# Performance work log

Measured on AMD Instinct MI355X. Metric: run time of the kernel, lower is better.

The kernel has to match this reference:

```python
import jax, jax.numpy as jnp
import numpy as np
from jax import lax

S, B, V, E, H = 512, 64, 50000, 400, 1150


def _lstm_layer(x, h0, c0, Wih, Whh, bih, bhh):
    # x: [S, B, Din]; PyTorch LSTM gate order: i, f, g, o
    WihT, WhhT = Wih.T, Whh.T

    def step(carry, xt):
        h, c = carry
        gates = xt @ WihT + bih + h @ WhhT + bhh  # [B, 4*Dh]
        i, f, g, o = jnp.split(gates, 4, axis=-1)
        c_new = jax.nn.sigmoid(f) * c + jax.nn.sigmoid(i) * jnp.tanh(g)
        h_new = jax.nn.sigmoid(o) * jnp.tanh(c_new)
        return (h_new, c_new), h_new

    (_, _), ys = lax.scan(step, (h0, c0), x)
    return ys  # [S, B, Dh]


def setup_inputs() -> dict:
    key = jax.random.key(0)

    def u(i, shape, s):
        return jax.random.uniform(jax.random.fold_in(key, i), shape, jnp.float32, -s, s)

    inp = {"tokens": jax.random.randint(jax.random.fold_in(key, 0), (S, B), 0, V)}
    inp["emb_w"] = u(1, (V, E), 0.1)  # encoder.weight.uniform_(-0.1, 0.1)
    dims = [(E, H), (H, H), (H, E)]  # (input_size, hidden_size) per layer
    k = 2
    for l, (din, dh) in enumerate(dims):
        s = 1.0 / float(np.sqrt(dh))
        inp[f"Wih{l}"] = u(k, (4 * dh, din), s); k += 1
        inp[f"Whh{l}"] = u(k, (4 * dh, dh), s); k += 1
        inp[f"bih{l}"] = u(k, (4 * dh,), s); k += 1
        inp[f"bhh{l}"] = u(k, (4 * dh,), s); k += 1
        inp[f"h{l}"] = jnp.zeros((B, dh), jnp.float32)
        inp[f"c{l}"] = jnp.zeros((B, dh), jnp.float32)
    return inp


def reference(tokens, emb_w, Wih0, Whh0, bih0, bhh0, Wih1, Whh1, bih1, bhh1,
              Wih2, Whh2, bih2, bhh2, h0, c0, h1, c1, h2, c2):
    # Eval-mode forward: embedding/locked/weight dropouts are identity.
    x = emb_w[tokens]  # [S, B, E]
    x = _lstm_layer(x, h0, c0, Wih0, Whh0, bih0, bhh0)  # [S, B, H]
    x = _lstm_layer(x, h1, c1, Wih1, Whh1, bih1, bhh1)  # [S, B, H]
    x = _lstm_layer(x, h2, c2, Wih2, Whh2, bih2, bhh2)  # [S, B, E]
    return x
```

## Files before the change

kernel.cpp:

```cpp
#include <hip/hip_runtime.h>
#include <hip/hip_bf16.h>
#include <cstdint>
#include <cstddef>


typedef _Float16 f16x8 __attribute__((ext_vector_type(8)));
typedef float f32x4 __attribute__((ext_vector_type(4)));
typedef unsigned int u32x4 __attribute__((ext_vector_type(4)));

#define LSTM_NBLK   241
#define LSTM_WSTEPS 515
#define LDS_W_HALFS (4 * 36 * 64 * 8)
#define LDS_TOTAL_BYTES (LDS_W_HALFS * 2 + 16384)
#define GO_BASE 248

struct KParams {
  const unsigned short* res[3];
  const unsigned short* strm[3];
  const float* bias[3];
  const unsigned short* xin0;
  unsigned short* hseq[3];
  float* part;
  float* out;
  int* bar;
};

__device__ __forceinline__ float sigm_(float x) { return 1.0f / (1.0f + __expf(-x)); }
__device__ __forceinline__ float tanh_(float x) { return 2.0f * sigm_(2.0f * x) - 1.0f; }
__device__ __forceinline__ unsigned short f2h(float x) {
  _Float16 h = (_Float16)x;
  return __builtin_bit_cast(unsigned short, h);
}
__device__ __forceinline__ f32x4 load_sc128f(const float* p) {
  f32x4 r;
  asm volatile("global_load_dwordx4 %0, %1, off sc0 sc1"
               : "=v"(r) : "v"(p) : "memory");
  return r;
}
__device__ __forceinline__ void store_sc128(unsigned short* p, u32x4 v) {
  asm volatile("global_store_dwordx4 %0, %1, off sc0 sc1" :: "v"(p), "v"(v) : "memory");
}
__device__ __forceinline__ void store_sc128f(float* p, f32x4 v) {
  asm volatile("global_store_dwordx4 %0, %1, off sc0 sc1" :: "v"(p), "v"(v) : "memory");
}
__device__ __forceinline__ void store_sc_i(int* p, int v) {
  asm volatile("global_store_dword %0, %1, off sc0 sc1" :: "v"(p), "v"(v) : "memory");
}
__device__ __forceinline__ int load_sc_i(const int* p) {
  int v;
  asm volatile("global_load_dword %0, %1, off sc0 sc1\n\ts_waitcnt vmcnt(0)"
               : "=v"(v) : "v"(p) : "memory");
  __builtin_amdgcn_sched_barrier(0);
  return v;
}
__device__ __forceinline__ void wait_vm0() {
  asm volatile("s_waitcnt vmcnt(0)" ::: "memory");
  __builtin_amdgcn_sched_barrier(0);
}

__device__ __forceinline__ void grid_barrier(int* bar, int bid, int tid, int tau1) {
  wait_vm0();
  __syncthreads();
  if (bid == 0) {
    if (tid >= 1 && tid < LSTM_NBLK) {
      int guard = 0;
      while (load_sc_i(&bar[tid * 32]) < tau1 && ++guard < (1 << 20))
        __builtin_amdgcn_s_sleep(1);
    }
    __syncthreads();
    if (tid < 8) store_sc_i(&bar[(GO_BASE + tid) * 32], tau1);
  } else {
    if (tid == 0) {
      store_sc_i(&bar[bid * 32], tau1);
      int guard = 0;
      while (load_sc_i(&bar[(GO_BASE + (bid & 7)) * 32]) < tau1 && ++guard < (1 << 20))
        __builtin_amdgcn_s_sleep(1);
    }
    __syncthreads();
  }
}

template<int L, int LAG>
__device__ __forceinline__ void run_layer(const KParams& p, int g, int bid,
                                          unsigned short* ldsW, float* gates) {
  constexpr int DH    = (L == 2) ? 400 : 1150;
  constexpr int NKB1  = (L == 0) ? 13 : 36;
  constexpr int NKB2  = (L == 2) ? 13 : 36;
  constexpr int XSTR  = (L == 0) ? 416 : 1152;
  constexpr int HSTR  = (L == 2) ? 416 : 1152;
  constexpr bool B1_RES = (L == 2);
  constexpr int NKB_ST = B1_RES ? NKB2 : NKB1;

  const unsigned short* __restrict__ strm = p.strm[L] + (size_t)g * (4 * NKB_ST * 512);
  const float* __restrict__ bias          = p.bias[L];
  const unsigned short* __restrict__ xin  = (L == 0) ? p.xin0 : p.hseq[L - 1];
  unsigned short* __restrict__ own        = p.hseq[L];

  const int tid  = threadIdx.x;
  const int lane = tid & 63;
  const int w    = tid >> 6;
  const int m0   = (w >> 2) << 4;
  const int kq   = w & 3;
  const int r    = lane & 15;
  const int q    = lane >> 4;

  {
    const uint4* src = (const uint4*)(p.res[L] + (size_t)g * LDS_W_HALFS);
    uint4* dst = (uint4*)ldsW;
    for (int i = tid; i < LDS_W_HALFS / 8; i += 1024) dst[i] = src[i];
#pragma unroll
    for (int s2 = 0; s2 < 4; ++s2) gates[s2 * 1024 + tid] = 0.0f;
  }

  const int b_ = tid >> 4;
  const int jp = tid & 15;
  const int jglob = g * 16 + jp;
  float bias4[4];
#pragma unroll
  for (int ss = 0; ss < 4; ++ss) bias4[ss] = bias[ss * 1152 + jglob];
  float c_val = 0.0f;
  __syncthreads();

  for (int tau = 0; tau < LSTM_WSTEPS; ++tau) {
    const int t = tau - LAG;
    if (t >= 0 && t < 512) {
      f32x4 acc[4] = {{0,0,0,0},{0,0,0,0},{0,0,0,0},{0,0,0,0}};

      const size_t slot1 = (L == 0) ? (size_t)t : (size_t)(t + 1);
      const unsigned short* a1base = xin + slot1 * (64 * XSTR) + (size_t)(m0 + r) * XSTR + q * 8;
      const unsigned short* a2base = own + (size_t)t * (64 * HSTR) + (size_t)(m0 + r) * HSTR + q * 8;

      f16x8 a1r[9]; f16x8 a2r[9];
      if constexpr (L != 0) {
#pragma unroll
        for (int i = 0; i < 9; ++i) {
          int kb = kq + 4 * i;
          if (NKB1 == 36 || kb < NKB1) a1r[i] = *(const f16x8*)(a1base + kb * 32);
        }
      }
#pragma unroll
      for (int i = 0; i < 9; ++i) {
        int kb = kq + 4 * i;
        if (i < ((NKB2 == 36) ? 9 : 4) && (NKB2 == 36 || kb < NKB2))
          a2r[i] = *(const f16x8*)(a2base + kb * 32);
      }

#pragma unroll
      for (int i = 0; i < ((NKB1 == 36) ? 9 : 4); ++i) {
        int kb = kq + 4 * i;
        if (NKB1 == 36 || kb < NKB1) {
          f16x8 a = (L == 0) ? *(const f16x8*)(a1base + kb * 32) : a1r[i];
#pragma unroll
          for (int s2 = 0; s2 < 4; ++s2) {
            f16x8 b = B1_RES
              ? *(const f16x8*)&ldsW[((s2 * 36 + kb) * 64 + lane) * 8]
              : *(const f16x8*)&strm[((size_t)(s2 * NKB_ST + kb) * 64 + lane) * 8];
            acc[s2] = __builtin_amdgcn_mfma_f32_16x16x32_f16(a, b, acc[s2], 0, 0, 0);
          }
        }
      }
#pragma unroll
      for (int i = 0; i < ((NKB2 == 36) ? 9 : 4); ++i) {
        int kb = kq + 4 * i;
        if (NKB2 == 36 || kb < NKB2) {
          f16x8 a = a2r[i];
#pragma unroll
          for (int s2 = 0; s2 < 4; ++s2) {
            f16x8 b = B1_RES
              ? *(const f16x8*)&strm[((size_t)(s2 * NKB_ST + kb) * 64 + lane) * 8]
              : *(const f16x8*)&ldsW[((s2 * 36 + kb) * 64 + lane) * 8];
            acc[s2] = __builtin_amdgcn_mfma_f32_16x16x32_f16(a, b, acc[s2], 0, 0, 0);
          }
        }
      }

#pragma unroll
      for (int s2 = 0; s2 < 4; ++s2)
#pragma unroll
        for (int i = 0; i < 4; ++i)
          atomicAdd(&gates[s2 * 1024 + (m0 + q * 4 + i) * 16 + r], acc[s2][i]);
      __syncthreads();

      float pg[4];
#pragma unroll
      for (int s2 = 0; s2 < 4; ++s2) {
        pg[s2] = gates[s2 * 1024 + tid];
        gates[s2 * 1024 + tid] = 0.0f;
      }
      float ig = sigm_(pg[0] + bias4[0]);
      float fg = sigm_(pg[1] + bias4[1]);
      float gg = tanh_(pg[2] + bias4[2]);
      float og = sigm_(pg[3] + bias4[3]);
      c_val = fg * c_val + ig * gg;
      float h = og * tanh_(c_val);
      if (jglob >= DH) h = 0.0f;

      unsigned v0  = (unsigned)f2h(h);
      unsigned o1  = __shfl_down(v0, 1);
      unsigned p01 = v0 | (o1 << 16);
      unsigned o2  = __shfl_down(p01, 2);
      unsigned o4a = __shfl_down(p01, 4);
      unsigned o4b = __shfl_down(o2, 4);
      if ((lane & 7) == 0) {
        u32x4 pk; pk[0] = p01; pk[1] = o2; pk[2] = o4a; pk[3] = o4b;
        store_sc128(own + ((size_t)(t + 1) * 64 + b_) * HSTR + jglob, pk);
      }
      if (L == 2 && jglob < DH)
        p.out[((size_t)t * 64 + b_) * 400 + jglob] = h;
    }
    grid_barrier(p.bar, bid, tid, tau + 1);
  }
}

__device__ __forceinline__ void run_l1_ih(const KParams& p, int g, int bid,
                                          unsigned short* ldsW, float* gates) {
  const unsigned short* __restrict__ xin = p.hseq[0];
  const int tid  = threadIdx.x;
  const int lane = tid & 63;
  const int w    = tid >> 6;
  const int m0   = (w >> 2) << 4;
  const int kq   = w & 3;
  const int r    = lane & 15;
  const int q    = lane >> 4;

  {
    const uint4* src = (const uint4*)(p.strm[1] + (size_t)g * LDS_W_HALFS);
    uint4* dst = (uint4*)ldsW;
    for (int i = tid; i < LDS_W_HALFS / 8; i += 1024) dst[i] = src[i];
#pragma unroll
    for (int s2 = 0; s2 < 4; ++s2) gates[s2 * 1024 + tid] = 0.0f;
  }
  __syncthreads();

  for (int tau = 0; tau < LSTM_WSTEPS; ++tau) {
    const int t = tau - 1;
    if (t >= 0 && t < 512) {
      f32x4 acc[4] = {{0,0,0,0},{0,0,0,0},{0,0,0,0},{0,0,0,0}};
      const unsigned short* a1base =
          xin + (size_t)(t + 1) * (64 * 1152) + (size_t)(m0 + r) * 1152 + q * 8;
      f16x8 a1r[9];
#pragma unroll
      for (int i = 0; i < 9; ++i) a1r[i] = *(const f16x8*)(a1base + (kq + 4 * i) * 32);
#pragma unroll
      for (int i = 0; i < 9; ++i) {
        int kb = kq + 4 * i;
        f16x8 a = a1r[i];
#pragma unroll
        for (int s2 = 0; s2 < 4; ++s2) {
          f16x8 b = *(const f16x8*)&ldsW[((s2 * 36 + kb) * 64 + lane) * 8];
          acc[s2] = __builtin_amdgcn_mfma_f32_16x16x32_f16(a, b, acc[s2], 0, 0, 0);
        }
      }
#pragma unroll
      for (int s2 = 0; s2 < 4; ++s2)
#pragma unroll
        for (int i = 0; i < 4; ++i)
          atomicAdd(&gates[s2 * 1024 + (m0 + q * 4 + i) * 16 + r], acc[s2][i]);
      __syncthreads();
      f32x4 pk;
#pragma unroll
      for (int s2 = 0; s2 < 4; ++s2) {
        pk[s2] = gates[s2 * 1024 + tid];
        gates[s2 * 1024 + tid] = 0.0f;
      }
      store_sc128f(p.part + ((size_t)((t & 1) * 72 + g) * 1024 + tid) * 4, pk);
    }
    grid_barrier(p.bar, bid, tid, tau + 1);
  }
}

__device__ __forceinline__ void run_l1_hh(const KParams& p, int g, int bid,
                                          unsigned short* ldsW, float* gates) {
  unsigned short* __restrict__ own = p.hseq[1];
  const int tid  = threadIdx.x;
  const int lane = tid & 63;
  const int w    = tid >> 6;
  const int m0   = (w >> 2) << 4;
  const int kq   = w & 3;
  const int r    = lane & 15;
  const int q    = lane >> 4;

  {
    const uint4* src = (const uint4*)(p.res[1] + (size_t)g * LDS_W_HALFS);
    uint4* dst = (uint4*)ldsW;
    for (int i = tid; i < LDS_W_HALFS / 8; i += 1024) dst[i] = src[i];
#pragma unroll
    for (int s2 = 0; s2 < 4; ++s2) gates[s2 * 1024 + tid] = 0.0f;
  }

  const int b_ = tid >> 4;
  const int jp = tid & 15;
  const int jglob = g * 16 + jp;
  float bias4[4];
#pragma unroll
  for (int ss = 0; ss < 4; ++ss) bias4[ss] = p.bias[1][ss * 1152 + jglob];
  float c_val = 0.0f;
  __syncthreads();

  for (int tau = 0; tau < LSTM_WSTEPS; ++tau) {
    const int t = tau - 2;
    if (t >= 0 && t < 512) {
      f32x4 acc[4] = {{0,0,0,0},{0,0,0,0},{0,0,0,0},{0,0,0,0}};
      const unsigned short* a2base =
          own + (size_t)t * (64 * 1152) + (size_t)(m0 + r) * 1152 + q * 8;
      f16x8 a2r[9];
#pragma unroll
      for (int i = 0; i < 9; ++i) a2r[i] = *(const f16x8*)(a2base + (kq + 4 * i) * 32);
      f32x4 pl = load_sc128f(p.part + ((size_t)((t & 1) * 72 + g) * 1024 + tid) * 4);
      wait_vm0();
#pragma unroll
      for (int i = 0; i < 9; ++i) {
        int kb = kq + 4 * i;
        f16x8 a = a2r[i];
#pragma unroll
        for (int s2 = 0; s2 < 4; ++s2) {
          f16x8 b = *(const f16x8*)&ldsW[((s2 * 36 + kb) * 64 + lane) * 8];
          acc[s2] = __builtin_amdgcn_mfma_f32_16x16x32_f16(a, b, acc[s2], 0, 0, 0);
        }
      }
#pragma unroll
      for (int s2 = 0; s2 < 4; ++s2)
#pragma unroll
        for (int i = 0; i < 4; ++i)
          atomicAdd(&gates[s2 * 1024 + (m0 + q * 4 + i) * 16 + r], acc[s2][i]);
      __syncthreads();

      float pg[4];
#pragma unroll
      for (int s2 = 0; s2 < 4; ++s2) {
        pg[s2] = gates[s2 * 1024 + tid];
        gates[s2 * 1024 + tid] = 0.0f;
      }
      float ig = sigm_(pg[0] + pl[0] + bias4[0]);
      float fg = sigm_(pg[1] + pl[1] + bias4[1]);
      float gg = tanh_(pg[2] + pl[2] + bias4[2]);
      float og = sigm_(pg[3] + pl[3] + bias4[3]);
      c_val = fg * c_val + ig * gg;
      float h = og * tanh_(c_val);
      if (jglob >= 1150) h = 0.0f;

      unsigned v0  = (unsigned)f2h(h);
      unsigned o1  = __shfl_down(v0, 1);
      unsigned p01 = v0 | (o1 << 16);
      unsigned o2  = __shfl_down(p01, 2);
      unsigned o4a = __shfl_down(p01, 4);
      unsigned o4b = __shfl_down(o2, 4);
      if ((lane & 7) == 0) {
        u32x4 pk2; pk2[0] = p01; pk2[1] = o2; pk2[2] = o4a; pk2[3] = o4b;
        store_sc128(own + ((size_t)(t + 1) * 64 + b_) * 1152 + jglob, pk2);
      }
    }
    grid_barrier(p.bar, bid, tid, tau + 1);
  }
}

__global__ void __launch_bounds__(1024) lstm_persistent(KParams p) {
  extern __shared__ unsigned short smem[];
  unsigned short* ldsW = smem;
  float* gates = (float*)(smem + LDS_W_HALFS);
  const int bid = blockIdx.x;
  if (bid < 72)       run_layer<0, 0>(p, bid, bid, ldsW, gates);
  else if (bid < 144) run_l1_ih(p, bid - 72, bid, ldsW, gates);
  else if (bid < 216) run_l1_hh(p, bid - 144, bid, ldsW, gates);
  else                run_layer<2, 3>(p, bid - 216, bid, ldsW, gates);
}

__global__ void prep_weights(const float* __restrict__ src,
                             unsigned short* __restrict__ dst,
                             int Jext, int jg, int K, int NKB) {
  const int n = jg * 4 * NKB * 512;
  for (int idx = blockIdx.x * blockDim.x + threadIdx.x; idx < n;
       idx += gridDim.x * blockDim.x) {
    int e = idx & 7;
    int t2 = idx >> 3;
    int ln = t2 & 63; t2 >>= 6;
    int kb = t2 % NKB; t2 /= NKB;
    int s = t2 & 3;
    int g = t2 >> 2;
    int j = g * 16 + (ln & 15);
    int k = kb * 32 + (ln >> 4) * 8 + e;
    unsigned short v = 0;
    if (j < Jext && k < K) v = f2h(src[(size_t)(s * Jext + j) * K + k]);
    dst[idx] = v;
  }
}

__global__ void prep_bias(const float* __restrict__ bih,
                          const float* __restrict__ bhh,
                          float* __restrict__ dst, int Dh) {
  const int n = 4 * 1152;
  for (int idx = blockIdx.x * blockDim.x + threadIdx.x; idx < n;
       idx += gridDim.x * blockDim.x) {
    int s = idx / 1152, j = idx % 1152;
    float v = 0.0f;
    if (j < Dh) v = bih[s * Dh + j] + bhh[s * Dh + j];
    dst[idx] = v;
  }
}

__global__ void prep_gather(const int* __restrict__ tokens,
                            const float* __restrict__ emb,
                            unsigned short* __restrict__ xin0) {
  const int n = 512 * 64 * 52;
  for (int idx = blockIdx.x * blockDim.x + threadIdx.x; idx < n;
       idx += gridDim.x * blockDim.x) {
    int row = idx / 52;
    int cp  = idx - row * 52;
    unsigned short v[8] = {0, 0, 0, 0, 0, 0, 0, 0};
    if (cp < 50) {
      const float* src = emb + (size_t)tokens[row] * 400 + cp * 8;
      float4 a = *(const float4*)(src);
      float4 b = *(const float4*)(src + 4);
      v[0] = f2h(a.x); v[1] = f2h(a.y); v[2] = f2h(a.z); v[3] = f2h(a.w);
      v[4] = f2h(b.x); v[5] = f2h(b.y); v[6] = f2h(b.z); v[7] = f2h(b.w);
    }
    *(uint4*)(xin0 + (size_t)row * 416 + cp * 8) = *(const uint4*)v;
  }
}

extern "C" void kernel_launch(void* const* d_in, const int* in_sizes, int n_in,
                              void* d_out, int out_size, void* d_ws, size_t ws_size,
                              hipStream_t stream) {
  const int*   tokens = (const int*)d_in[0];
  const float* emb  = (const float*)d_in[1];
  const float* Wih0 = (const float*)d_in[2];
  const float* Whh0 = (const float*)d_in[3];
  const float* bih0 = (const float*)d_in[4];
  const float* bhh0 = (const float*)d_in[5];
  const float* Wih1 = (const float*)d_in[8];
  const float* Whh1 = (const float*)d_in[9];
  const float* bih1 = (const float*)d_in[10];
  const float* bhh1 = (const float*)d_in[11];
  const float* Wih2 = (const float*)d_in[14];
  const float* Whh2 = (const float*)d_in[15];
  const float* bih2 = (const float*)d_in[16];
  const float* bhh2 = (const float*)d_in[17];

  char* ws = (char*)d_ws;
  size_t off = 0;
  auto alloc = [&](size_t bytes) -> char* {
    char* ptr = ws + off;
    off += (bytes + 255) & ~(size_t)255;
    return ptr;
  };
  unsigned short* res0  = (unsigned short*)alloc(72ull * 4 * 36 * 512 * 2);
  unsigned short* res1  = (unsigned short*)alloc(72ull * 4 * 36 * 512 * 2);
  unsigned short* res2  = (unsigned short*)alloc(25ull * 4 * 36 * 512 * 2);
  unsigned short* strm0 = (unsigned short*)alloc(72ull * 4 * 13 * 512 * 2);
  unsigned short* strm1 = (unsigned short*)alloc(72ull * 4 * 36 * 512 * 2);
  unsigned short* strm2 = (unsigned short*)alloc(25ull * 4 * 13 * 512 * 2);
  float* bias0 = (float*)alloc(4ull * 1152 * 4);
  float* bias1 = (float*)alloc(4ull * 1152 * 4);
  float* bias2 = (float*)alloc(4ull * 1152 * 4);
  unsigned short* xin0  = (unsigned short*)alloc(512ull * 64 * 416 * 2);
  unsigned short* hseq0 = (unsigned short*)alloc(513ull * 64 * 1152 * 2);
  unsigned short* hseq1 = (unsigned short*)alloc(513ull * 64 * 1152 * 2);
  unsigned short* hseq2 = (unsigned short*)alloc(513ull * 64 * 416 * 2);
  float* part = (float*)alloc(2ull * 72 * 1024 * 4 * 4);
  int* bar = (int*)alloc((GO_BASE + 8) * 32 * 4);
  if (off > ws_size) return;

  hipLaunchKernelGGL(prep_gather, dim3(2048), dim3(256), 0, stream, tokens, emb, xin0);
  hipLaunchKernelGGL(prep_weights, dim3(4096), dim3(256), 0, stream, Whh0, res0, 1150, 72, 1150, 36);
  hipLaunchKernelGGL(prep_weights, dim3(4096), dim3(256), 0, stream, Whh1, res1, 1150, 72, 1150, 36);
  hipLaunchKernelGGL(prep_weights, dim3(4096), dim3(256), 0, stream, Wih2, res2, 400, 25, 1150, 36);
  hipLaunchKernelGGL(prep_weights, dim3(4096), dim3(256), 0, stream, Wih0, strm0, 1150, 72, 400, 13);
  hipLaunchKernelGGL(prep_weights, dim3(4096), dim3(256), 0, stream, Wih1, strm1, 1150, 72, 1150, 36);
  hipLaunchKernelGGL(prep_weights, dim3(4096), dim3(256), 0, stream, Whh2, strm2, 400, 25, 400, 13);
  hipLaunchKernelGGL(prep_bias, dim3(8), dim3(256), 0, stream, bih0, bhh0, bias0, 1150);
  hipLaunchKernelGGL(prep_bias, dim3(8), dim3(256), 0, stream, bih1, bhh1, bias1, 1150);
  hipLaunchKernelGGL(prep_bias, dim3(8), dim3(256), 0, stream, bih2, bhh2, bias2, 400);
  (void)hipMemsetAsync(hseq0, 0, 64ull * 1152 * 2, stream);
  (void)hipMemsetAsync(hseq1, 0, 64ull * 1152 * 2, stream);
  (void)hipMemsetAsync(hseq2, 0, 64ull * 416 * 2, stream);
  (void)hipMemsetAsync(bar, 0, (GO_BASE + 8) * 32 * 4, stream);

  KParams kp;
  kp.res[0] = res0;  kp.res[1] = res1;  kp.res[2] = res2;
  kp.strm[0] = strm0; kp.strm[1] = strm1; kp.strm[2] = strm2;
  kp.bias[0] = bias0; kp.bias[1] = bias1; kp.bias[2] = bias2;
  kp.xin0 = xin0;
  kp.hseq[0] = hseq0; kp.hseq[1] = hseq1; kp.hseq[2] = hseq2;
  kp.part = part;
  kp.out = (float*)d_out;
  kp.bar = bar;

  (void)hipFuncSetAttribute((const void*)lstm_persistent,
                            hipFuncAttributeMaxDynamicSharedMemorySize,
                            LDS_TOTAL_BYTES);
  hipLaunchKernelGGL(lstm_persistent, dim3(LSTM_NBLK), dim3(1024),
                     LDS_TOTAL_BYTES, stream, kp);
}
```

Measured before the change: 15.26 ms.

## Halve block size and give each wave two M tiles to reuse B fragments

The persistent LSTM kernel drops from 1024 to 512 threads per block. Each wave now computes two 16-row batch tiles, so every weight fragment read from LDS or global memory feeds two MFMAs, and each thread handles two gate elements. The aim is to cut weight-fragment loads and LDS atomic traffic per timestep. In exchange there are fewer waves to hide latency in this latency-bound recurrent loop and more register pressure. The templated layer function is also split into dedicated layer-0 and layer-2 functions that preload the streamed B fragments.

New measurement: 16.02 ms. 1.05x slower.

```diff
diff --git a/kernel.cpp b/kernel.cpp
--- a/kernel.cpp
+++ b/kernel.cpp
@@ -10,6 +10,7 @@
 
 #define LSTM_NBLK   241
 #define LSTM_WSTEPS 515
+#define THREADS     512
 #define LDS_W_HALFS (4 * 36 * 64 * 8)
 #define LDS_TOTAL_BYTES (LDS_W_HALFS * 2 + 16384)
 #define GO_BASE 248
@@ -80,133 +81,146 @@
   }
 }
 
-template<int L, int LAG>
-__device__ __forceinline__ void run_layer(const KParams& p, int g, int bid,
-                                          unsigned short* ldsW, float* gates) {
-  constexpr int DH    = (L == 2) ? 400 : 1150;
-  constexpr int NKB1  = (L == 0) ? 13 : 36;
-  constexpr int NKB2  = (L == 2) ? 13 : 36;
-  constexpr int XSTR  = (L == 0) ? 416 : 1152;
-  constexpr int HSTR  = (L == 2) ? 416 : 1152;
-  constexpr bool B1_RES = (L == 2);
-  constexpr int NKB_ST = B1_RES ? NKB2 : NKB1;
-
-  const unsigned short* __restrict__ strm = p.strm[L] + (size_t)g * (4 * NKB_ST * 512);
-  const float* __restrict__ bias          = p.bias[L];
-  const unsigned short* __restrict__ xin  = (L == 0) ? p.xin0 : p.hseq[L - 1];
-  unsigned short* __restrict__ own        = p.hseq[L];
+template<bool HASP>
+__device__ __forceinline__ float lstm_ew(float* gates, int e, const float b4[4],
+                                         const f32x4* pl, float& c_val) {
+  float pg[4];
+#pragma unroll
+  for (int s2 = 0; s2 < 4; ++s2) {
+    pg[s2] = gates[s2 * 1024 + e];
+    gates[s2 * 1024 + e] = 0.0f;
+  }
+  float ig = sigm_(pg[0] + (HASP ? (*pl)[0] : 0.0f) + b4[0]);
+  float fg = sigm_(pg[1] + (HASP ? (*pl)[1] : 0.0f) + b4[1]);
+  float gg = tanh_(pg[2] + (HASP ? (*pl)[2] : 0.0f) + b4[2]);
+  float og = sigm_(pg[3] + (HASP ? (*pl)[3] : 0.0f) + b4[3]);
+  c_val = fg * c_val + ig * gg;
+  return og * tanh_(c_val);
+}
+
+__device__ __forceinline__ void pack_store16(unsigned short* base, int lane, float h) {
+  unsigned v0  = (unsigned)f2h(h);
+  unsigned o1  = __shfl_down(v0, 1);
+  unsigned p01 = v0 | (o1 << 16);
+  unsigned o2  = __shfl_down(p01, 2);
+  unsigned o4a = __shfl_down(p01, 4);
+  unsigned o4b = __shfl_down(o2, 4);
+  if ((lane & 7) == 0) {
+    u32x4 pk; pk[0] = p01; pk[1] = o2; pk[2] = o4a; pk[3] = o4b;
+    store_sc128(base, pk);
+  }
+}
+
+__device__ __forceinline__ void run_l0(const KParams& p, int g, int bid,
+                                       unsigned short* ldsW, float* gates) {
+  const unsigned short* __restrict__ strmA = p.strm[0] + (size_t)g * (4 * 13 * 512);
+  const unsigned short* __restrict__ xin   = p.xin0;
+  unsigned short* __restrict__ own         = p.hseq[0];
 
   const int tid  = threadIdx.x;
   const int lane = tid & 63;
   const int w    = tid >> 6;
-  const int m0   = (w >> 2) << 4;
   const int kq   = w & 3;
+  const int m0   = (w >> 2) * 32;
   const int r    = lane & 15;
   const int q    = lane >> 4;
 
   {
-    const uint4* src = (const uint4*)(p.res[L] + (size_t)g * LDS_W_HALFS);
+    const uint4* src = (const uint4*)(p.res[0] + (size_t)g * LDS_W_HALFS);
     uint4* dst = (uint4*)ldsW;
-    for (int i = tid; i < LDS_W_HALFS / 8; i += 1024) dst[i] = src[i];
-#pragma unroll
-    for (int s2 = 0; s2 < 4; ++s2) gates[s2 * 1024 + tid] = 0.0f;
-  }
-
-  const int b_ = tid >> 4;
+    for (int i = tid; i < LDS_W_HALFS / 8; i += THREADS) dst[i] = src[i];
+#pragma unroll
+    for (int s2 = 0; s2 < 4; ++s2) {
+      gates[s2 * 1024 + tid] = 0.0f;
+      gates[s2 * 1024 + tid + 512] = 0.0f;
+    }
+  }
   const int jp = tid & 15;
   const int jglob = g * 16 + jp;
   float bias4[4];
 #pragma unroll
-  for (int ss = 0; ss < 4; ++ss) bias4[ss] = bias[ss * 1152 + jglob];
-  float c_val = 0.0f;
+  for (int ss = 0; ss < 4; ++ss) bias4[ss] = p.bias[0][ss * 1152 + jglob];
+  float c0 = 0.0f, c1 = 0.0f;
   __syncthreads();
 
   for (int tau = 0; tau < LSTM_WSTEPS; ++tau) {
-    const int t = tau - LAG;
-    if (t >= 0 && t < 512) {
-      f32x4 acc[4] = {{0,0,0,0},{0,0,0,0},{0,0,0,0},{0,0,0,0}};
-
-      const size_t slot1 = (L == 0) ? (size_t)t : (size_t)(t + 1);
-      const unsigned short* a1base = xin + slot1 * (64 * XSTR) + (size_t)(m0 + r) * XSTR + q * 8;
-      const unsigned short* a2base = own + (size_t)t * (64 * HSTR) + (size_t)(m0 + r) * HSTR + q * 8;
-
-      f16x8 a1r[9]; f16x8 a2r[9];
-      if constexpr (L != 0) {
-#pragma unroll
-        for (int i = 0; i < 9; ++i) {
+    const int t = tau;
+    if (t < 512) {
+      f16x8 a2r[2][9];
+#pragma unroll
+      for (int mi = 0; mi < 2; ++mi) {
+        const unsigned short* a2b =
+            own + (size_t)t * (64 * 1152) + (size_t)(m0 + mi * 16 + r) * 1152 + q * 8;
+#pragma unroll
+        for (int i = 0; i < 9; ++i) a2r[mi][i] = *(const f16x8*)(a2b + (kq + 4 * i) * 32);
+      }
+      f16x8 a1r[2][4]; f16x8 bS[4][4];
+#pragma unroll
+      for (int mi = 0; mi < 2; ++mi) {
+        const unsigned short* a1b =
+            xin + ((size_t)t * 64 + (m0 + mi * 16 + r)) * 416 + q * 8;
+#pragma unroll
+        for (int i = 0; i < 4; ++i) {
           int kb = kq + 4 * i;
-          if (NKB1 == 36 || kb < NKB1) a1r[i] = *(const f16x8*)(a1base + kb * 32);
+          if (kb < 13) a1r[mi][i] = *(const f16x8*)(a1b + kb * 32);
+        }
+      }
+#pragma unroll
+      for (int i = 0; i < 4; ++i) {
+        int kb = kq + 4 * i;
+        if (kb < 13) {
+#pragma unroll
+          for (int s2 = 0; s2 < 4; ++s2)
+            bS[i][s2] = *(const f16x8*)&strmA[((size_t)(s2 * 13 + kb) * 64 + lane) * 8];
+        }
+      }
+
+      f32x4 acc[2][4];
+#pragma unroll
+      for (int mi = 0; mi < 2; ++mi)
+#pragma unroll
+        for (int s2 = 0; s2 < 4; ++s2) acc[mi][s2] = (f32x4){0, 0, 0, 0};
+
+#pragma unroll
+      for (int i = 0; i < 4; ++i) {
+        int kb = kq + 4 * i;
+        if (kb < 13) {
+#pragma unroll
+          for (int s2 = 0; s2 < 4; ++s2)
+#pragma unroll
+            for (int mi = 0; mi < 2; ++mi)
+              acc[mi][s2] = __builtin_amdgcn_mfma_f32_16x16x32_f16(
+                  a1r[mi][i], bS[i][s2], acc[mi][s2], 0, 0, 0);
         }
       }
 #pragma unroll
       for (int i = 0; i < 9; ++i) {
         int kb = kq + 4 * i;
-        if (i < ((NKB2 == 36) ? 9 : 4) && (NKB2 == 36 || kb < NKB2))
-          a2r[i] = *(const f16x8*)(a2base + kb * 32);
-      }
-
-#pragma unroll
-      for (int i = 0; i < ((NKB1 == 36) ? 9 : 4); ++i) {
-        int kb = kq + 4 * i;
-        if (NKB1 == 36 || kb < NKB1) {
-          f16x8 a = (L == 0) ? *(const f16x8*)(a1base + kb * 32) : a1r[i];
-#pragma unroll
-          for (int s2 = 0; s2 < 4; ++s2) {
-            f16x8 b = B1_RES
-              ? *(const f16x8*)&ldsW[((s2 * 36 + kb) * 64 + lane) * 8]
-              : *(const f16x8*)&strm[((size_t)(s2 * NKB_ST + kb) * 64 + lane) * 8];
-            acc[s2] = __builtin_amdgcn_mfma_f32_16x16x32_f16(a, b, acc[s2], 0, 0, 0);
-          }
-        }
-      }
-#pragma unroll
-      for (int i = 0; i < ((NKB2 == 36) ? 9 : 4); ++i) {
-        int kb = kq + 4 * i;
-        if (NKB2 == 36 || kb < NKB2) {
-          f16x8 a = a2r[i];
-#pragma unroll
-          for (int s2 = 0; s2 < 4; ++s2) {
-            f16x8 b = B1_RES
-              ? *(const f16x8*)&strm[((size_t)(s2 * NKB_ST + kb) * 64 + lane) * 8]
-              : *(const f16x8*)&ldsW[((s2 * 36 + kb) * 64 + lane) * 8];
-            acc[s2] = __builtin_amdgcn_mfma_f32_16x16x32_f16(a, b, acc[s2], 0, 0, 0);
-          }
-        }
-      }
-
-#pragma unroll
-      for (int s2 = 0; s2 < 4; ++s2)
-#pragma unroll
-        for (int i = 0; i < 4; ++i)
-          atomicAdd(&gates[s2 * 1024 + (m0 + q * 4 + i) * 16 + r], acc[s2][i]);
+#pragma unroll
+        for (int s2 = 0; s2 < 4; ++s2) {
+          f16x8 b = *(const f16x8*)&ldsW[((s2 * 36 + kb) * 64 + lane) * 8];
+#pragma unroll
+          for (int mi = 0; mi < 2; ++mi)
+            acc[mi][s2] = __builtin_amdgcn_mfma_f32_16x16x32_f16(
+                a2r[mi][i], b, acc[mi][s2], 0, 0, 0);
+        }
+      }
+#pragma unroll
+      for (int mi = 0; mi < 2; ++mi)
+#pragma unroll
+        for (int s2 = 0; s2 < 4; ++s2)
+#pragma unroll
+          for (int i = 0; i < 4; ++i)
+            atomicAdd(&gates[s2 * 1024 + (m0 + mi * 16 + q * 4 + i) * 16 + r],
+                      acc[mi][s2][i]);
       __syncthreads();
 
-      float pg[4];
-#pragma unroll
-      for (int s2 = 0; s2 < 4; ++s2) {
-        pg[s2] = gates[s2 * 1024 + tid];
-        gates[s2 * 1024 + tid] = 0.0f;
-      }
-      float ig = sigm_(pg[0] + bias4[0]);
-      float fg = sigm_(pg[1] + bias4[1]);
-      float gg = tanh_(pg[2] + bias4[2]);
-      float og = sigm_(pg[3] + bias4[3]);
-      c_val = fg * c_val + ig * gg;
-      float h = og * tanh_(c_val);
-      if (jglob >= DH) h = 0.0f;
-
-      unsigned v0  = (unsigned)f2h(h);
-      unsigned o1  = __shfl_down(v0, 1);
-      unsigned p01 = v0 | (o1 << 16);
-      unsigned o2  = __shfl_down(p01, 2);
-      unsigned o4a = __shfl_down(p01, 4);
-      unsigned o4b = __shfl_down(o2, 4);
-      if ((lane & 7) == 0) {
-        u32x4 pk; pk[0] = p01; pk[1] = o2; pk[2] = o4a; pk[3] = o4b;
-        store_sc128(own + ((size_t)(t + 1) * 64 + b_) * HSTR + jglob, pk);
-      }
-      if (L == 2 && jglob < DH)
-        p.out[((size_t)t * 64 + b_) * 400 + jglob] = h;
+      float h0 = lstm_ew<false>(gates, tid, bias4, nullptr, c0);
+      float h1 = lstm_ew<false>(gates, tid + 512, bias4, nullptr, c1);
+      if (jglob >= 1150) { h0 = 0.0f; h1 = 0.0f; }
+      const int b0 = tid >> 4, b1 = b0 + 32;
+      pack_store16(own + ((size_t)(t + 1) * 64 + b0) * 1152 + jglob, lane, h0);
+      pack_store16(own + ((size_t)(t + 1) * 64 + b1) * 1152 + jglob, lane, h1);
     }
     grid_barrier(p.bar, bid, tid, tau + 1);
   }
@@ -218,52 +232,70 @@
   const int tid  = threadIdx.x;
   const int lane = tid & 63;
   const int w    = tid >> 6;
-  const int m0   = (w >> 2) << 4;
   const int kq   = w & 3;
+  const int m0   = (w >> 2) * 32;
   const int r    = lane & 15;
   const int q    = lane >> 4;
 
   {
     const uint4* src = (const uint4*)(p.strm[1] + (size_t)g * LDS_W_HALFS);
     uint4* dst = (uint4*)ldsW;
-    for (int i = tid; i < LDS_W_HALFS / 8; i += 1024) dst[i] = src[i];
-#pragma unroll
-    for (int s2 = 0; s2 < 4; ++s2) gates[s2 * 1024 + tid] = 0.0f;
+    for (int i = tid; i < LDS_W_HALFS / 8; i += THREADS) dst[i] = src[i];
+#pragma unroll
+    for (int s2 = 0; s2 < 4; ++s2) {
+      gates[s2 * 1024 + tid] = 0.0f;
+      gates[s2 * 1024 + tid + 512] = 0.0f;
+    }
   }
   __syncthreads();
 
   for (int tau = 0; tau < LSTM_WSTEPS; ++tau) {
     const int t = tau - 1;
     if (t >= 0 && t < 512) {
-      f32x4 acc[4] = {{0,0,0,0},{0,0,0,0},{0,0,0,0},{0,0,0,0}};
-      const unsigned short* a1base =
-          xin + (size_t)(t + 1) * (64 * 1152) + (size_t)(m0 + r) * 1152 + q * 8;
-      f16x8 a1r[9];
-#pragma unroll
-      for (int i = 0; i < 9; ++i) a1r[i] = *(const f16x8*)(a1base + (kq + 4 * i) * 32);
+      f16x8 a1r[2][9];
+#pragma unroll
+      for (int mi = 0; mi < 2; ++mi) {
+        const unsigned short* a1b =
+            xin + (size_t)(t + 1) * (64 * 1152) + (size_t)(m0 + mi * 16 + r) * 1152 + q * 8;
+#pragma unroll
+        for (int i = 0; i < 9; ++i) a1r[mi][i] = *(const f16x8*)(a1b + (kq + 4 * i) * 32);
+      }
+      f32x4 acc[2][4];
+#pragma unroll
+      for (int mi = 0; mi < 2; ++mi)
+#pragma unroll
+        for (int s2 = 0; s2 < 4; ++s2) acc[mi][s2] = (f32x4){0, 0, 0, 0};
 #pragma unroll
       for (int i = 0; i < 9; ++i) {
         int kb = kq + 4 * i;
-        f16x8 a = a1r[i];
 #pragma unroll
         for (int s2 = 0; s2 < 4; ++s2) {
           f16x8 b = *(const f16x8*)&ldsW[((s2 * 36 + kb) * 64 + lane) * 8];
-          acc[s2] = __builtin_amdgcn_mfma_f32_16x16x32_f16(a, b, acc[s2], 0, 0, 0);
-        }
-      }
-#pragma unroll
-      for (int s2 = 0; s2 < 4; ++s2)
-#pragma unroll
-        for (int i = 0; i < 4; ++i)
-          atomicAdd(&gates[s2 * 1024 + (m0 + q * 4 + i) * 16 + r], acc[s2][i]);
+#pragma unroll
+          for (int mi = 0; mi < 2; ++mi)
+            acc[mi][s2] = __builtin_amdgcn_mfma_f32_16x16x32_f16(
+                a1r[mi][i], b, acc[mi][s2], 0, 0, 0);
+        }
+      }
+#pragma unroll
+      for (int mi = 0; mi < 2; ++mi)
+#pragma unroll
+        for (int s2 = 0; s2 < 4; ++s2)
+#pragma unroll
+          for (int i = 0; i < 4; ++i)
+            atomicAdd(&gates[s2 * 1024 + (m0 + mi * 16 + q * 4 + i) * 16 + r],
+                      acc[mi][s2][i]);
       __syncthreads();
-      f32x4 pk;
+
+      f32x4 pk0, pk1;
 #pragma unroll
       for (int s2 = 0; s2 < 4; ++s2) {
-        pk[s2] = gates[s2 * 1024 + tid];
-        gates[s2 * 1024 + tid] = 0.0f;
-      }
-      store_sc128f(p.part + ((size_t)((t & 1) * 72 + g) * 1024 + tid) * 4, pk);
+        pk0[s2] = gates[s2 * 1024 + tid];       gates[s2 * 1024 + tid] = 0.0f;
+        pk1[s2] = gates[s2 * 1024 + tid + 512]; gates[s2 * 1024 + tid + 512] = 0.0f;
+      }
+      float* pb = p.part + (size_t)((t & 1) * 72 + g) * 1024 * 4;
+      store_sc128f(pb + (size_t)tid * 4, pk0);
+      store_sc128f(pb + (size_t)(tid + 512) * 4, pk1);
     }
     grid_barrier(p.bar, bid, tid, tau + 1);
   }
@@ -275,94 +307,212 @@
   const int tid  = threadIdx.x;
   const int lane = tid & 63;
   const int w    = tid >> 6;
-  const int m0   = (w >> 2) << 4;
   const int kq   = w & 3;
+  const int m0   = (w >> 2) * 32;
   const int r    = lane & 15;
   const int q    = lane >> 4;
 
   {
     const uint4* src = (const uint4*)(p.res[1] + (size_t)g * LDS_W_HALFS);
     uint4* dst = (uint4*)ldsW;
-    for (int i = tid; i < LDS_W_HALFS / 8; i += 1024) dst[i] = src[i];
-#pragma unroll
-    for (int s2 = 0; s2 < 4; ++s2) gates[s2 * 1024 + tid] = 0.0f;
-  }
-
-  const int b_ = tid >> 4;
+    for (int i = tid; i < LDS_W_HALFS / 8; i += THREADS) dst[i] = src[i];
+#pragma unroll
+    for (int s2 = 0; s2 < 4; ++s2) {
+      gates[s2 * 1024 + tid] = 0.0f;
+      gates[s2 * 1024 + tid + 512] = 0.0f;
+    }
+  }
   const int jp = tid & 15;
   const int jglob = g * 16 + jp;
   float bias4[4];
 #pragma unroll
   for (int ss = 0; ss < 4; ++ss) bias4[ss] = p.bias[1][ss * 1152 + jglob];
-  float c_val = 0.0f;
+  float c0 = 0.0f, c1 = 0.0f;
   __syncthreads();
 
   for (int tau = 0; tau < LSTM_WSTEPS; ++tau) {
     const int t = tau - 2;
     if (t >= 0 && t < 512) {
-      f32x4 acc[4] = {{0,0,0,0},{0,0,0,0},{0,0,0,0},{0,0,0,0}};
-      const unsigned short* a2base =
-          own + (size_t)t * (64 * 1152) + (size_t)(m0 + r) * 1152 + q * 8;
-      f16x8 a2r[9];
-#pragma unroll
-      for (int i = 0; i < 9; ++i) a2r[i] = *(const f16x8*)(a2base + (kq + 4 * i) * 32);
-      f32x4 pl = load_sc128f(p.part + ((size_t)((t & 1) * 72 + g) * 1024 + tid) * 4);
+      f16x8 a2r[2][9];
+#pragma unroll
+      for (int mi = 0; mi < 2; ++mi) {
+        const unsigned short* a2b =
+            own + (size_t)t * (64 * 1152) + (size_t)(m0 + mi * 16 + r) * 1152 + q * 8;
+#pragma unroll
+        for (int i = 0; i < 9; ++i) a2r[mi][i] = *(const f16x8*)(a2b + (kq + 4 * i) * 32);
+      }
+      const float* pb = p.part + (size_t)((t & 1) * 72 + g) * 1024 * 4;
+      f32x4 pl0 = load_sc128f(pb + (size_t)tid * 4);
+      f32x4 pl1 = load_sc128f(pb + (size_t)(tid + 512) * 4);
       wait_vm0();
+
+      f32x4 acc[2][4];
+#pragma unroll
+      for (int mi = 0; mi < 2; ++mi)
+#pragma unroll
+        for (int s2 = 0; s2 < 4; ++s2) acc[mi][s2] = (f32x4){0, 0, 0, 0};
 #pragma unroll
       for (int i = 0; i < 9; ++i) {
         int kb = kq + 4 * i;
-        f16x8 a = a2r[i];
 #pragma unroll
         for (int s2 = 0; s2 < 4; ++s2) {
           f16x8 b = *(const f16x8*)&ldsW[((s2 * 36 + kb) * 64 + lane) * 8];
-          acc[s2] = __builtin_amdgcn_mfma_f32_16x16x32_f16(a, b, acc[s2], 0, 0, 0);
-        }
-      }
-#pragma unroll
-      for (int s2 = 0; s2 < 4; ++s2)
-#pragma unroll
-        for (int i = 0; i < 4; ++i)
-          atomicAdd(&gates[s2 * 1024 + (m0 + q * 4 + i) * 16 + r], acc[s2][i]);
+#pragma unroll
+          for (int mi = 0; mi < 2; ++mi)
+            acc[mi][s2] = __builtin_amdgcn_mfma_f32_16x16x32_f16(
+                a2r[mi][i], b, acc[mi][s2], 0, 0, 0);
+        }
+      }
+#pragma unroll
+      for (int mi = 0; mi < 2; ++mi)
+#pragma unroll
+        for (int s2 = 0; s2 < 4; ++s2)
+#pragma unroll
+          for (int i = 0; i < 4; ++i)
+            atomicAdd(&gates[s2 * 1024 + (m0 + mi * 16 + q * 4 + i) * 16 + r],
+                      acc[mi][s2][i]);
       __syncthreads();
 
-      float pg[4];
-#pragma unroll
-      for (int s2 = 0; s2 < 4; ++s2) {
-        pg[s2] = gates[s2 * 1024 + tid];
-        gates[s2 * 1024 + tid] = 0.0f;
-      }
-      float ig = sigm_(pg[0] + pl[0] + bias4[0]);
-      float fg = sigm_(pg[1] + pl[1] + bias4[1]);
-      float gg = tanh_(pg[2] + pl[2] + bias4[2]);
-      float og = sigm_(pg[3] + pl[3] + bias4[3]);
-      c_val = fg * c_val + ig * gg;
-      float h = og * tanh_(c_val);
-      if (jglob >= 1150) h = 0.0f;
-
-      unsigned v0  = (unsigned)f2h(h);
-      unsigned o1  = __shfl_down(v0, 1);
-      unsigned p01 = v0 | (o1 << 16);
-      unsigned o2  = __shfl_down(p01, 2);
-      unsigned o4a = __shfl_down(p01, 4);
-      unsigned o4b = __shfl_down(o2, 4);
-      if ((lane & 7) == 0) {
-        u32x4 pk2; pk2[0] = p01; pk2[1] = o2; pk2[2] = o4a; pk2[3] = o4b;
-        store_sc128(own + ((size_t)(t + 1) * 64 + b_) * 1152 + jglob, pk2);
-      }
+      float h0 = lstm_ew<true>(gates, tid, bias4, &pl0, c0);
+      float h1 = lstm_ew<true>(gates, tid + 512, bias4, &pl1, c1);
+      if (jglob >= 1150) { h0 = 0.0f; h1 = 0.0f; }
+      const int b0 = tid >> 4, b1 = b0 + 32;
+      pack_store16(own + ((size_t)(t + 1) * 64 + b0) * 1152 + jglob, lane, h0);
+      pack_store16(own + ((size_t)(t + 1) * 64 + b1) * 1152 + jglob, lane, h1);
     }
     grid_barrier(p.bar, bid, tid, tau + 1);
   }
 }
 
-__global__ void __launch_bounds__(1024) lstm_persistent(KParams p) {
+__device__ __forceinline__ void run_l2(const KParams& p, int g, int bid,
+                                       unsigned short* ldsW, float* gates) {
+  const unsigned short* __restrict__ strmB = p.strm[2] + (size_t)g * (4 * 13 * 512);
+  const unsigned short* __restrict__ xin   = p.hseq[1];
+  unsigned short* __restrict__ own         = p.hseq[2];
+
+  const int tid  = threadIdx.x;
+  const int lane = tid & 63;
+  const int w    = tid >> 6;
+  const int kq   = w & 3;
+  const int m0   = (w >> 2) * 32;
+  const int r    = lane & 15;
+  const int q    = lane >> 4;
+
+  {
+    const uint4* src = (const uint4*)(p.res[2] + (size_t)g * LDS_W_HALFS);
+    uint4* dst = (uint4*)ldsW;
+    for (int i = tid; i < LDS_W_HALFS / 8; i += THREADS) dst[i] = src[i];
+#pragma unroll
+    for (int s2 = 0; s2 < 4; ++s2) {
+      gates[s2 * 1024 + tid] = 0.0f;
+      gates[s2 * 1024 + tid + 512] = 0.0f;
+    }
+  }
+  const int jp = tid & 15;
+  const int jglob = g * 16 + jp;
+  float bias4[4];
+#pragma unroll
+  for (int ss = 0; ss < 4; ++ss) bias4[ss] = p.bias[2][ss * 1152 + jglob];
+  float c0 = 0.0f, c1 = 0.0f;
+  __syncthreads();
+
+  for (int tau = 0; tau < LSTM_WSTEPS; ++tau) {
+    const int t = tau - 3;
+    if (t >= 0 && t < 512) {
+      f16x8 a1r[2][9];
+#pragma unroll
+      for (int mi = 0; mi < 2; ++mi) {
+        const unsigned short* a1b =
+            xin + (size_t)(t + 1) * (64 * 1152) + (size_t)(m0 + mi * 16 + r) * 1152 + q * 8;
+#pragma unroll
+        for (int i = 0; i < 9; ++i) a1r[mi][i] = *(const f16x8*)(a1b + (kq + 4 * i) * 32);
+      }
+      f16x8 a2r[2][4];
+#pragma unroll
+      for (int mi = 0; mi < 2; ++mi) {
+        const unsigned short* a2b =
+            own + (size_t)t * (64 * 416) + (size_t)(m0 + mi * 16 + r) * 416 + q * 8;
+#pragma unroll
+        for (int i = 0; i < 4; ++i) {
+          int kb = kq + 4 * i;
+          if (kb < 13) a2r[mi][i] = *(const f16x8*)(a2b + kb * 32);
+        }
+      }
+      f16x8 bS[4][4];
+#pragma unroll
+      for (int i = 0; i < 4; ++i) {
+        int kb = kq + 4 * i;
+        if (kb < 13) {
+#pragma unroll
+          for (int s2 = 0; s2 < 4; ++s2)
+            bS[i][s2] = *(const f16x8*)&strmB[((size_t)(s2 * 13 + kb) * 64 + lane) * 8];
+        }
+      }
+
+      f32x4 acc[2][4];
+#pragma unroll
+      for (int mi = 0; mi < 2; ++mi)
+#pragma unroll
+        for (int s2 = 0; s2 < 4; ++s2) acc[mi][s2] = (f32x4){0, 0, 0, 0};
+
+#pragma unroll
+      for (int i = 0; i < 9; ++i) {
+        int kb = kq + 4 * i;
+#pragma unroll
+        for (int s2 = 0; s2 < 4; ++s2) {
+          f16x8 b = *(const f16x8*)&ldsW[((s2 * 36 + kb) * 64 + lane) * 8];
+#pragma unroll
+          for (int mi = 0; mi < 2; ++mi)
+            acc[mi][s2] = __builtin_amdgcn_mfma_f32_16x16x32_f16(
+                a1r[mi][i], b, acc[mi][s2], 0, 0, 0);
+        }
+      }
+#pragma unroll
+      for (int i = 0; i < 4; ++i) {
+        int kb = kq + 4 * i;
+        if (kb < 13) {
+#pragma unroll
+          for (int s2 = 0; s2 < 4; ++s2)
+#pragma unroll
+            for (int mi = 0; mi < 2; ++mi)
+              acc[mi][s2] = __builtin_amdgcn_mfma_f32_16x16x32_f16(
+                  a2r[mi][i], bS[i][s2], acc[mi][s2], 0, 0, 0);
+        }
+      }
+#pragma unroll
+      for (int mi = 0; mi < 2; ++mi)
+#pragma unroll
+        for (int s2 = 0; s2 < 4; ++s2)
+#pragma unroll
+          for (int i = 0; i < 4; ++i)
+            atomicAdd(&gates[s2 * 1024 + (m0 + mi * 16 + q * 4 + i) * 16 + r],
+                      acc[mi][s2][i]);
+      __syncthreads();
+
+      float h0 = lstm_ew<false>(gates, tid, bias4, nullptr, c0);
+      float h1 = lstm_ew<false>(gates, tid + 512, bias4, nullptr, c1);
+      if (jglob >= 400) { h0 = 0.0f; h1 = 0.0f; }
+      const int b0 = tid >> 4, b1 = b0 + 32;
+      pack_store16(own + ((size_t)(t + 1) * 64 + b0) * 416 + jglob, lane, h0);
+      pack_store16(own + ((size_t)(t + 1) * 64 + b1) * 416 + jglob, lane, h1);
+      if (jglob < 400) {
+        p.out[((size_t)t * 64 + b0) * 400 + jglob] = h0;
+        p.out[((size_t)t * 64 + b1) * 400 + jglob] = h1;
+      }
+    }
+    grid_barrier(p.bar, bid, tid, tau + 1);
+  }
+}
+
+__global__ void __launch_bounds__(THREADS, 2) lstm_persistent(KParams p) {
   extern __shared__ unsigned short smem[];
   unsigned short* ldsW = smem;
   float* gates = (float*)(smem + LDS_W_HALFS);
   const int bid = blockIdx.x;
-  if (bid < 72)       run_layer<0, 0>(p, bid, bid, ldsW, gates);
+  if (bid < 72)       run_l0(p, bid, bid, ldsW, gates);
   else if (bid < 144) run_l1_ih(p, bid - 72, bid, ldsW, gates);
   else if (bid < 216) run_l1_hh(p, bid - 144, bid, ldsW, gates);
-  else                run_layer<2, 3>(p, bid - 216, bid, ldsW, gates);
+  else                run_l2(p, bid - 216, bid, ldsW, gates);
 }
 
 __global__ void prep_weights(const float* __restrict__ src,
@@ -488,6 +638,6 @@
   (void)hipFuncSetAttribute((const void*)lstm_persistent,
                             hipFuncAttributeMaxDynamicSharedMemorySize,
                             LDS_TOTAL_BYTES);
-  hipLaunchKernelGGL(lstm_persistent, dim3(LSTM_NBLK), dim3(1024),
+  hipLaunchKernelGGL(lstm_persistent, dim3(LSTM_NBLK), dim3(THREADS),
                      LDS_TOTAL_BYTES, stream, kp);
 }
```
